# Kernel tuning notes

Hardware: AMD Instinct MI355X
Metric: run time of the kernel (lower is better)

Reference implementation:

```python
import jax, jax.numpy as jnp
import numpy as np

N = 50000          # nodes
E = 800000         # edges (avg degree 16)
T = 4              # edge types (edge_attr_dim)
H = 8              # heads
C1 = 16            # state_dim (per-head channels, layer 1)
C2 = 8             # out_dim  (per-head channels, layer 2)
D = 128            # node_attr_dim
NEG = -1e9         # masked-attention logit
LRELU_SLOPE = 0.2  # PyG GATConv default negative_slope


def setup_inputs() -> dict:
    key = jax.random.key(0)
    ks = jax.random.split(key, 12)
    x = jax.random.normal(ks[0], (N, D), jnp.float32)
    edge_src = jax.random.randint(ks[1], (E,), 0, N, jnp.int32)
    edge_dst = jax.random.randint(ks[2], (E,), 0, N, jnp.int32)
    edge_type = jax.random.randint(ks[3], (E,), 0, T, jnp.int32)
    W1 = jax.random.normal(ks[4], (T, D, H * C1), jnp.float32) * (1.0 / np.sqrt(D))
    a1_src = jax.random.normal(ks[5], (T, H, C1), jnp.float32) * 0.1
    a1_dst = jax.random.normal(ks[6], (T, H, C1), jnp.float32) * 0.1
    b1 = jnp.zeros((T, H * C1), jnp.float32)
    W2 = jax.random.normal(ks[7], (T, H * C1, H * C2), jnp.float32) * (1.0 / np.sqrt(H * C1))
    a2_src = jax.random.normal(ks[8], (T, H, C2), jnp.float32) * 0.1
    a2_dst = jax.random.normal(ks[9], (T, H, C2), jnp.float32) * 0.1
    b2 = jnp.zeros((T, H * C2), jnp.float32)
    return dict(x=x, edge_src=edge_src, edge_dst=edge_dst, edge_type=edge_type,
                W1=W1, a1_src=a1_src, a1_dst=a1_dst, b1=b1,
                W2=W2, a2_src=a2_src, a2_dst=a2_dst, b2=b2)


def gat_conv(x_in, W, a_src, a_dst, b, src, dst, mask, n):
    """One PyG-style GATConv (concat heads, eval mode) on masked edge list."""
    heads, c = a_src.shape
    h = (x_in @ W).reshape(n, heads, c)                       # [N,H,C]
    s_src = jnp.sum(h * a_src, axis=-1)                        # [N,H]
    s_dst = jnp.sum(h * a_dst, axis=-1)                        # [N,H]
    e = jax.nn.leaky_relu(s_src[src] + s_dst[dst], LRELU_SLOPE)  # [Et,H]
    e = jnp.where(mask[:, None], e, NEG)
    m = jax.ops.segment_max(e, dst, num_segments=n)            # [N,H]
    p = jnp.exp(e - m[dst]) * mask[:, None].astype(e.dtype)    # unnorm softmax
    denom = jax.ops.segment_sum(p, dst, num_segments=n)        # [N,H]
    msg = p[:, :, None] * h[src]                               # [Et,H,C]
    agg = jax.ops.segment_sum(msg, dst, num_segments=n)        # [N,H,C]
    out = agg / denom[:, :, None]
    return out.reshape(n, heads * c) + b


def reference(x, edge_src, edge_dst, edge_type, W1, a1_src, a1_dst, b1,
              W2, a2_src, a2_dst, b2):
    n = x.shape[0]
    loops = jnp.arange(n, dtype=edge_src.dtype)
    src = jnp.concatenate([edge_src, loops])   # self-loops appended (PyG default)
    dst = jnp.concatenate([edge_dst, loops])
    ones = jnp.ones((n,), bool)
    outs = []
    for t in range(T):
        mask = jnp.concatenate([edge_type == t, ones])
        h1 = gat_conv(x, W1[t], a1_src[t], a1_dst[t], b1[t], src, dst, mask, n)
        h1 = jax.nn.relu(h1)
        h2 = gat_conv(h1, W2[t], a2_src[t], a2_dst[t], b2[t], src, dst, mask, n)
        outs.append(h2)
    return jnp.concatenate(outs, axis=1)       # [N, T*H*C2]
```

## Files before the change

### kernel.cpp

```cpp
#include <hip/hip_runtime.h>
#include <cstddef>

constexpr int NN  = 50000;
constexpr int NE  = 800000;
constexpr int NT  = 4;
constexpr int NH  = 8;
constexpr int C1  = 16;
constexpr int C2  = 8;
constexpr int DD  = 128;
constexpr int HC1 = NH * C1;
constexpr int HC2 = NH * C2;
constexpr int CAP = 22;
constexpr int BSTRIDE = 48;
constexpr float SLOPE = 0.2f;

constexpr int G_ZERO = 2344;
constexpr int G_P1   = NT * 16384 / 256;
constexpr int G_P2   = NT * 8192 / 256;
constexpr int G_SCAT = 782;
constexpr int G_GEMM = (NN + 63) / 64;
constexpr int G_GAT1 = NN / 16;
constexpr int G_GAT2 = (NN + 31) / 32;

using short8 = __attribute__((ext_vector_type(8))) short;
using f32x4  = __attribute__((ext_vector_type(4))) float;
typedef unsigned short u16;
typedef unsigned char  u8;

__device__ __forceinline__ float lrelu(float x) { return x > 0.f ? x : SLOPE * x; }
__device__ __forceinline__ float bfl(unsigned u) { return __uint_as_float(u << 16); }
__device__ __forceinline__ float bfh(unsigned u) { return __uint_as_float(u & 0xffff0000u); }
__device__ __forceinline__ u16 f2bf(float f) {
    unsigned u = __float_as_uint(f);
    return (u16)((u + 0x7fffu + ((u >> 16) & 1u)) >> 16);
}
__device__ __forceinline__ void deci8(uint2 v, float sc, float f[8]) {
    int w0 = (int)v.x, w1 = (int)v.y;
    f[0] = (float)((w0 << 24) >> 24) * sc;
    f[1] = (float)((w0 << 16) >> 24) * sc;
    f[2] = (float)((w0 <<  8) >> 24) * sc;
    f[3] = (float)( w0        >> 24) * sc;
    f[4] = (float)((w1 << 24) >> 24) * sc;
    f[5] = (float)((w1 << 16) >> 24) * sc;
    f[6] = (float)((w1 <<  8) >> 24) * sc;
    f[7] = (float)( w1        >> 24) * sc;
}
__device__ __forceinline__ float dotf(const float h[8], const float* a) {
    return h[0]*a[0] + h[1]*a[1] + h[2]*a[2] + h[3]*a[3]
         + h[4]*a[4] + h[5]*a[5] + h[6]*a[6] + h[7]*a[7];
}
__device__ __forceinline__ float dot8(uint4 hv, const float* a) {
    return bfl(hv.x) * a[0] + bfh(hv.x) * a[1] + bfl(hv.y) * a[2] + bfh(hv.y) * a[3]
         + bfl(hv.z) * a[4] + bfh(hv.z) * a[5] + bfl(hv.w) * a[6] + bfh(hv.w) * a[7];
}
__device__ __forceinline__ unsigned qperm(unsigned own, unsigned part, unsigned sel) {
    return __builtin_amdgcn_perm(own, part, sel);
}

__device__ __forceinline__ void scatter4(int e0, const int* __restrict__ esrc,
        const int* __restrict__ edst, const int* __restrict__ etyp,
        unsigned* __restrict__ bkt, int tmin, int tmax) {
    int bk[4], src[4];
    bool v[4];
    #pragma unroll
    for (int k = 0; k < 4; ++k) {
        int i = e0 + k * 256;
        bk[k] = 0; src[k] = 0;
        v[k] = false;
        if (i < NE) {
            int ty = etyp[i];
            v[k] = (ty >= tmin) && (ty <= tmax);
            if (v[k]) { bk[k] = ty * NN + edst[i]; src[k] = esrc[i]; }
        }
    }
    int slot[4];
    #pragma unroll
    for (int k = 0; k < 4; ++k)
        if (v[k]) slot[k] = atomicAdd((int*)((char*)bkt + (size_t)bk[k] * BSTRIDE), 1);
    #pragma unroll
    for (int k = 0; k < 4; ++k)
        if (v[k] && slot[k] < CAP)
            ((u16*)((char*)bkt + (size_t)bk[k] * BSTRIDE))[2 + slot[k]] = (u16)src[k];
}

__global__ __launch_bounds__(256) void init_kernel(const float* __restrict__ W1,
        u16* __restrict__ wp1, const float* __restrict__ W2, u16* __restrict__ wp2,
        unsigned* __restrict__ bkt) {
    const int b = blockIdx.x, tid = threadIdx.x;
    if (b < G_ZERO) {
        int i = b * 256 + tid;
        if (i < 600000) reinterpret_cast<uint4*>(bkt)[i] = make_uint4(0, 0, 0, 0);
    } else if (b < G_ZERO + G_P1) {
        int i = (b - G_ZERO) * 256 + tid;
        int t = i >> 14, r = i & 16383;
        int ntl = r >> 11, ks = (r >> 9) & 3, lane = (r >> 3) & 63, j = r & 7;
        int col = ntl * 16 + (lane & 15);
        int k   = ks * 32 + (lane >> 4) * 8 + j;
        wp1[i] = f2bf(W1[((size_t)t * DD + k) * HC1 + col]);
    } else {
        int i = (b - G_ZERO - G_P1) * 256 + tid;
        int t = i >> 13, r = i & 8191;
        int ntl = r >> 11, ks = (r >> 9) & 3, lane = (r >> 3) & 63, j = r & 7;
        int col = ntl * 16 + (lane & 15);
        int k   = ks * 32 + (lane >> 4) * 8 + j;
        wp2[i] = f2bf(W2[((size_t)t * HC1 + k) * HC2 + col]);
    }
}

__global__ __launch_bounds__(256) void scat_kernel(const int* __restrict__ esrc,
        const int* __restrict__ edst, const int* __restrict__ etyp,
        unsigned* __restrict__ bkt, int t) {
    scatter4(blockIdx.x * 1024 + threadIdx.x, esrc, edst, etyp, bkt, t, t);
}

__global__ __launch_bounds__(256) void gemm_kernel(const float* __restrict__ x,
        const u16* __restrict__ wp1, u8* __restrict__ h1, float* __restrict__ sc1) {
    constexpr int NTILE = HC1 / 16;
    const int bx = blockIdx.x, tid = threadIdx.x;
    const int wave = tid >> 6;
    const int lane = tid & 63;
    const int q    = lane >> 4;
    const int c    = lane & 15;
    const int rowbase = bx * 64 + wave * 16;

    int arow = rowbase + c; if (arow >= NN) arow = NN - 1;
    short8 afrag[4];
    const float* xp = x + (size_t)arow * DD + q * 8;
    #pragma unroll
    for (int ks = 0; ks < 4; ++ks) {
        float4 f0 = *reinterpret_cast<const float4*>(xp + ks * 32);
        float4 f1 = *reinterpret_cast<const float4*>(xp + ks * 32 + 4);
        short8 a;
        a[0] = (short)f2bf(f0.x); a[1] = (short)f2bf(f0.y);
        a[2] = (short)f2bf(f0.z); a[3] = (short)f2bf(f0.w);
        a[4] = (short)f2bf(f1.x); a[5] = (short)f2bf(f1.y);
        a[6] = (short)f2bf(f1.z); a[7] = (short)f2bf(f1.w);
        afrag[ks] = a;
    }

    for (int t = 0; t < 4; ++t) {
        f32x4 acc[NTILE];
        #pragma unroll
        for (int ntl = 0; ntl < NTILE; ++ntl) acc[ntl] = (f32x4){0.f, 0.f, 0.f, 0.f};
        const short8* wp = reinterpret_cast<const short8*>(wp1 + (size_t)t * 16384) + lane;
        #pragma unroll
        for (int ntl = 0; ntl < NTILE; ++ntl)
            #pragma unroll
            for (int ks = 0; ks < 4; ++ks) {
                short8 b = wp[(ntl * 4 + ks) * 64];
                acc[ntl] = __builtin_amdgcn_mfma_f32_16x16x32_bf16(afrag[ks], b, acc[ntl], 0, 0, 0);
            }

        float mx[NTILE][4];
        #pragma unroll
        for (int ntl = 0; ntl < NTILE; ++ntl)
            #pragma unroll
            for (int reg = 0; reg < 4; ++reg) mx[ntl][reg] = fabsf(acc[ntl][reg]);
        #pragma unroll
        for (int m = 1; m < 16; m <<= 1)
            #pragma unroll
            for (int ntl = 0; ntl < NTILE; ++ntl)
                #pragma unroll
                for (int reg = 0; reg < 4; ++reg)
                    mx[ntl][reg] = fmaxf(mx[ntl][reg], __shfl_xor(mx[ntl][reg], m));

        u8*    h1w = h1  + (size_t)t * NN * HC1;
        float* scw = sc1 + (size_t)t * NN * 8;

        #pragma unroll
        for (int reg = 0; reg < 4; ++reg) {
            int row = rowbase + q * 4 + reg;
            unsigned w0 = 0, w1 = 0;
            #pragma unroll
            for (int ntl = 0; ntl < 4; ++ntl) {
                float m = mx[ntl][reg];
                float rs = m > 0.f ? 127.f / m : 0.f;
                int iv = __float2int_rn(acc[ntl][reg] * rs);
                w0 |= ((unsigned)iv & 0xffu) << (8 * ntl);
            }
            #pragma unroll
            for (int ntl = 4; ntl < 8; ++ntl) {
                float m = mx[ntl][reg];
                float rs = m > 0.f ? 127.f / m : 0.f;
                int iv = __float2int_rn(acc[ntl][reg] * rs);
                w1 |= ((unsigned)iv & 0xffu) << (8 * (ntl - 4));
            }
            unsigned sel1 = (c & 1) ? 0x07030501u : 0x02060004u;
            unsigned p0 = __shfl_xor(w0, 1), p1 = __shfl_xor(w1, 1);
            w0 = qperm(w0, p0, sel1);
            w1 = qperm(w1, p1, sel1);
            unsigned sel2 = (c & 2) ? 0x07060302u : 0x01000504u;
            p0 = __shfl_xor(w0, 2); p1 = __shfl_xor(w1, 2);
            w0 = qperm(w0, p0, sel2);
            w1 = qperm(w1, p1, sel2);
            if (row < NN) {
                unsigned* rp = reinterpret_cast<unsigned*>(h1w + (size_t)row * HC1);
                rp[(c & 3) * 4 + (c >> 2)]       = w0;
                rp[((c & 3) + 4) * 4 + (c >> 2)] = w1;
            }
        }
        {
            int reg = c >> 2, hp = c & 3;
            int row = rowbase + q * 4 + reg;
            if (row < NN) {
                float2 s;
                s.x = mx[2 * hp][reg] * (1.f / 127.f);
                s.y = mx[2 * hp + 1][reg] * (1.f / 127.f);
                reinterpret_cast<float2*>(scw)[(size_t)row * 4 + hp] = s;
            }
        }
    }
}

template<int TPN, bool SPLIT, bool I8>
__device__ __forceinline__ void gather_body(const unsigned* __restrict__ bkt, int bk,
        int q, const float* asr, float sdn, const void* __restrict__ hbase,
        const float* __restrict__ scp, float& den, float acc[8]) {
    const uint2* bp = reinterpret_cast<const uint2*>((const char*)bkt + (size_t)bk * BSTRIDE);
    unsigned w[12];
    #pragma unroll
    for (int i = 0; i < 6; ++i) { uint2 u = bp[i]; w[2 * i] = u.x; w[2 * i + 1] = u.y; }
    int deg = (int)w[0]; if (deg > CAP) deg = CAP;
    #pragma unroll
    for (int c = 0; c < 6; ++c) {
        if (c * 4 >= deg) break;
        unsigned lo = w[1 + 2 * c];
        unsigned hi = (c < 5) ? w[2 + 2 * c] : 0u;
        int sv[4] = {(int)(lo & 0xffff), (int)(lo >> 16),
                     (int)(hi & 0xffff), (int)(hi >> 16)};
        #pragma unroll
        for (int j = 0; j < 4; ++j) {
            if (c * 4 + j < deg) {
                int sn = sv[j];
                float hf[8];
                if constexpr (I8) {
                    uint2 hv = reinterpret_cast<const uint2*>(hbase)[(size_t)sn * TPN + q];
                    float sc = scp[(size_t)sn * 8 + (q >> 1)];
                    deci8(hv, sc, hf);
                } else {
                    uint4 hv = reinterpret_cast<const uint4*>(hbase)[(size_t)sn * TPN + q];
                    hf[0] = bfl(hv.x); hf[1] = bfh(hv.x);
                    hf[2] = bfl(hv.y); hf[3] = bfh(hv.y);
                    hf[4] = bfl(hv.z); hf[5] = bfh(hv.z);
                    hf[6] = bfl(hv.w); hf[7] = bfh(hv.w);
                }
                float d = dotf(hf, asr);
                if (SPLIT) d += __shfl_xor(d, 1);
                float pp = __expf(lrelu(d + sdn));
                den += pp;
                #pragma unroll
                for (int i = 0; i < 8; ++i) acc[i] += pp * hf[i];
            }
        }
    }
}

__global__ __launch_bounds__(256) void g1g2_kernel(const unsigned* __restrict__ bkt,
        int t, const u8* __restrict__ h1r, const float* __restrict__ sc1r,
        const float* __restrict__ a1s_t, const float* __restrict__ a1d_t,
        const float* __restrict__ b1t, const u16* __restrict__ wp2t,
        u16* __restrict__ h2w) {
    const int bx = blockIdx.x, tid = threadIdx.x;
    __shared__ u16 lt[16][136];
    const int node0 = bx * 16;
    const int nl    = tid >> 4;
    const int node  = node0 + nl;
    const int q     = tid & 15;
    const int head  = q >> 1;
    const int bk    = t * NN + node;

    float asr[8], adr[8];
    #pragma unroll
    for (int i = 0; i < 8; ++i) {
        asr[i] = a1s_t[head * C1 + (q & 1) * 8 + i];
        adr[i] = a1d_t[head * C1 + (q & 1) * 8 + i];
    }

    uint2 hv = reinterpret_cast<const uint2*>(h1r)[(size_t)node * 16 + q];
    float scn = sc1r[(size_t)node * 8 + head];
    float hs[8];
    deci8(hv, scn, hs);
    float ds = dotf(hs, asr); ds += __shfl_xor(ds, 1);
    float dd = dotf(hs, adr); dd += __shfl_xor(dd, 1);
    const float sdn = dd;

    float p = __expf(lrelu(ds + sdn));
    float den = p;
    float acc[8];
    #pragma unroll
    for (int i = 0; i < 8; ++i) acc[i] = p * hs[i];
    gather_body<16, true, true>(bkt, bk, q, asr, sdn, h1r, sc1r, den, acc);

    float inv = 1.f / den;
    uint4 ov;
    {
        float o[8];
        #pragma unroll
        for (int i = 0; i < 8; ++i)
            o[i] = fmaxf(acc[i] * inv + b1t[q * 8 + i], 0.f);
        ov.x = (unsigned)f2bf(o[0]) | ((unsigned)f2bf(o[1]) << 16);
        ov.y = (unsigned)f2bf(o[2]) | ((unsigned)f2bf(o[3]) << 16);
        ov.z = (unsigned)f2bf(o[4]) | ((unsigned)f2bf(o[5]) << 16);
        ov.w = (unsigned)f2bf(o[6]) | ((unsigned)f2bf(o[7]) << 16);
    }
    *reinterpret_cast<uint4*>(&lt[nl][q * 8]) = ov;
    __syncthreads();

    const int wave = tid >> 6;
    const int lane = tid & 63;
    const int quad = lane >> 4;
    const int c    = lane & 15;
    short8 af[4];
    #pragma unroll
    for (int ks = 0; ks < 4; ++ks)
        af[ks] = *reinterpret_cast<const short8*>(&lt[c][ks * 32 + quad * 8]);
    f32x4 cacc = (f32x4){0.f, 0.f, 0.f, 0.f};
    const short8* wp = reinterpret_cast<const short8*>(wp2t) + lane;
    #pragma unroll
    for (int ks = 0; ks < 4; ++ks)
        cacc = __builtin_amdgcn_mfma_f32_16x16x32_bf16(af[ks], wp[(wave * 4 + ks) * 64], cacc, 0, 0, 0);

    const int col = wave * 16 + c;
    #pragma unroll
    for (int reg = 0; reg < 4; ++reg) {
        int row = node0 + quad * 4 + reg;
        h2w[(size_t)row * HC2 + col] = f2bf(cacc[reg]);
    }
}

__global__ __launch_bounds__(256) void gat2_kernel(const unsigned* __restrict__ bkt,
        int t, const u16* __restrict__ h2r, const float* __restrict__ a2s_t,
        const float* __restrict__ a2d_t, const float* __restrict__ b2t,
        float* __restrict__ out) {
    const int bx = blockIdx.x, tid = threadIdx.x;
    const int node = bx * 32 + (tid >> 3);
    if (node >= NN) return;
    const int q    = tid & 7;
    const int head = q;
    const int bk   = t * NN + node;
    const uint4* __restrict__ h4 = reinterpret_cast<const uint4*>(h2r);

    float asr[8], adr[8];
    #pragma unroll
    for (int i = 0; i < 8; ++i) {
        asr[i] = a2s_t[head * C2 + i];
        adr[i] = a2d_t[head * C2 + i];
    }

    uint4 hv = h4[(size_t)node * 8 + q];
    const float sdn = dot8(hv, adr);
    float p = __expf(lrelu(dot8(hv, asr) + sdn));
    float den = p;
    float acc[8];
    acc[0] = p * bfl(hv.x); acc[1] = p * bfh(hv.x);
    acc[2] = p * bfl(hv.y); acc[3] = p * bfh(hv.y);
    acc[4] = p * bfl(hv.z); acc[5] = p * bfh(hv.z);
    acc[6] = p * bfl(hv.w); acc[7] = p * bfh(hv.w);
    gather_body<8, false, false>(bkt, bk, q, asr, sdn, h2r, nullptr, den, acc);

    float inv = 1.f / den;
    float o[8];
    #pragma unroll
    for (int i = 0; i < 8; ++i) o[i] = acc[i] * inv + b2t[q * 8 + i];
    float* op = out + (size_t)node * (NT * HC2) + t * HC2 + q * 8;
    reinterpret_cast<float4*>(op)[0] = make_float4(o[0], o[1], o[2], o[3]);
    reinterpret_cast<float4*>(op)[1] = make_float4(o[4], o[5], o[6], o[7]);
}

extern "C" void kernel_launch(void* const* d_in, const int* in_sizes, int n_in,
                              void* d_out, int out_size, void* d_ws, size_t ws_size,
                              hipStream_t stream) {
    const float* x    = (const float*)d_in[0];
    const int*   esrc = (const int*)d_in[1];
    const int*   edst = (const int*)d_in[2];
    const int*   etyp = (const int*)d_in[3];
    const float* W1   = (const float*)d_in[4];
    const float* a1s  = (const float*)d_in[5];
    const float* a1d  = (const float*)d_in[6];
    const float* b1   = (const float*)d_in[7];
    const float* W2   = (const float*)d_in[8];
    const float* a2s  = (const float*)d_in[9];
    const float* a2d  = (const float*)d_in[10];
    const float* b2   = (const float*)d_in[11];
    float* out = (float*)d_out;
    char* base = (char*)d_ws;

    u8*    h1  = (u8*)base;
    float* sc1 = (float*)(base + 25600000);
    u16*   h2d[2] = {(u16*)(base + 32000000), (u16*)(base + 38400000)};
    unsigned* bkt = (unsigned*)(base + 44800000);
    u16* wp1 = (u16*)(base + 54400000);
    u16* wp2 = (u16*)(base + 54531072);

    dim3 blk(256);
    hipLaunchKernelGGL(init_kernel, dim3(G_ZERO + G_P1 + G_P2), blk, 0, stream,
                       W1, wp1, W2, wp2, bkt);
    for (int t = 0; t < 4; ++t)
        hipLaunchKernelGGL(scat_kernel, dim3(G_SCAT), blk, 0, stream,
                           esrc, edst, etyp, bkt, t);
    hipLaunchKernelGGL(gemm_kernel, dim3(G_GEMM), blk, 0, stream,
                       x, wp1, h1, sc1);

    auto g1g2 = [&](int t) {
        hipLaunchKernelGGL(g1g2_kernel, dim3(G_GAT1), blk, 0, stream,
                           bkt, t, h1 + (size_t)t * NN * HC1, sc1 + (size_t)t * NN * 8,
                           a1s + t * NH * C1, a1d + t * NH * C1, b1 + t * HC1,
                           wp2 + (size_t)t * 8192, h2d[t & 1]);
    };
    auto gat2 = [&](int t) {
        hipLaunchKernelGGL(gat2_kernel, dim3(G_GAT2), blk, 0, stream,
                           bkt, t, h2d[t & 1], a2s + t * NH * C2, a2d + t * NH * C2,
                           b2 + t * HC2, out);
    };
    g1g2(0); g1g2(1); gat2(0); g1g2(2); gat2(1); g1g2(3); gat2(2); gat2(3);
}
```

Measured before the change: 320.7 us.

## Split GEMM across edge types per wave with LDS-staged x and coalesced int8 stores

The layer-1 projection kernel now handles 16 rows per block, and each of the four waves computes one edge type in parallel. Before, each wave handled 16 rows and looped over all four types. The x tile is converted to bf16 once into shared memory and shared by all waves. Quantized int8 outputs are staged in LDS so each wave writes full 16-byte coalesced stores instead of scattered 4-byte ones. This adds a barrier and LDS traffic, quadruples the block count, and drops the row bounds checks because 50000 is divisible by 16.

```diff
diff --git a/kernel.cpp b/kernel.cpp
--- a/kernel.cpp
+++ b/kernel.cpp
@@ -18,7 +18,7 @@
 constexpr int G_P1   = NT * 16384 / 256;
 constexpr int G_P2   = NT * 8192 / 256;
 constexpr int G_SCAT = 782;
-constexpr int G_GEMM = (NN + 63) / 64;
+constexpr int G_GEMM = NN / 16;
 constexpr int G_GAT1 = NN / 16;
 constexpr int G_GAT2 = (NN + 31) / 32;
 
@@ -116,99 +116,105 @@
 __global__ __launch_bounds__(256) void gemm_kernel(const float* __restrict__ x,
         const u16* __restrict__ wp1, u8* __restrict__ h1, float* __restrict__ sc1) {
     constexpr int NTILE = HC1 / 16;
+    __shared__ u16 xls[16][136];
+    __shared__ unsigned st[4][16][36];
     const int bx = blockIdx.x, tid = threadIdx.x;
-    const int wave = tid >> 6;
+    const int w    = tid >> 6;
     const int lane = tid & 63;
     const int q    = lane >> 4;
     const int c    = lane & 15;
-    const int rowbase = bx * 64 + wave * 16;
-
-    int arow = rowbase + c; if (arow >= NN) arow = NN - 1;
+    const int rowbase = bx * 16;
+
+    {
+        int r = tid >> 4, g8 = tid & 15;
+        const float4* xp = reinterpret_cast<const float4*>(
+            x + (size_t)(rowbase + r) * DD + g8 * 8);
+        float4 f0 = xp[0], f1 = xp[1];
+        uint4 o;
+        o.x = (unsigned)f2bf(f0.x) | ((unsigned)f2bf(f0.y) << 16);
+        o.y = (unsigned)f2bf(f0.z) | ((unsigned)f2bf(f0.w) << 16);
+        o.z = (unsigned)f2bf(f1.x) | ((unsigned)f2bf(f1.y) << 16);
+        o.w = (unsigned)f2bf(f1.z) | ((unsigned)f2bf(f1.w) << 16);
+        *reinterpret_cast<uint4*>(&xls[r][g8 * 8]) = o;
+    }
+    __syncthreads();
+
     short8 afrag[4];
-    const float* xp = x + (size_t)arow * DD + q * 8;
-    #pragma unroll
-    for (int ks = 0; ks < 4; ++ks) {
-        float4 f0 = *reinterpret_cast<const float4*>(xp + ks * 32);
-        float4 f1 = *reinterpret_cast<const float4*>(xp + ks * 32 + 4);
-        short8 a;
-        a[0] = (short)f2bf(f0.x); a[1] = (short)f2bf(f0.y);
-        a[2] = (short)f2bf(f0.z); a[3] = (short)f2bf(f0.w);
-        a[4] = (short)f2bf(f1.x); a[5] = (short)f2bf(f1.y);
-        a[6] = (short)f2bf(f1.z); a[7] = (short)f2bf(f1.w);
-        afrag[ks] = a;
-    }
-
-    for (int t = 0; t < 4; ++t) {
-        f32x4 acc[NTILE];
-        #pragma unroll
-        for (int ntl = 0; ntl < NTILE; ++ntl) acc[ntl] = (f32x4){0.f, 0.f, 0.f, 0.f};
-        const short8* wp = reinterpret_cast<const short8*>(wp1 + (size_t)t * 16384) + lane;
+    #pragma unroll
+    for (int ks = 0; ks < 4; ++ks)
+        afrag[ks] = *reinterpret_cast<const short8*>(&xls[c][q * 8 + ks * 32]);
+
+    f32x4 acc[NTILE];
+    #pragma unroll
+    for (int ntl = 0; ntl < NTILE; ++ntl) acc[ntl] = (f32x4){0.f, 0.f, 0.f, 0.f};
+    const short8* wp = reinterpret_cast<const short8*>(wp1 + (size_t)w * 16384) + lane;
+    #pragma unroll
+    for (int ntl = 0; ntl < NTILE; ++ntl)
+        #pragma unroll
+        for (int ks = 0; ks < 4; ++ks) {
+            short8 b = wp[(ntl * 4 + ks) * 64];
+            acc[ntl] = __builtin_amdgcn_mfma_f32_16x16x32_bf16(afrag[ks], b, acc[ntl], 0, 0, 0);
+        }
+
+    float mx[NTILE][4];
+    #pragma unroll
+    for (int ntl = 0; ntl < NTILE; ++ntl)
+        #pragma unroll
+        for (int reg = 0; reg < 4; ++reg) mx[ntl][reg] = fabsf(acc[ntl][reg]);
+    #pragma unroll
+    for (int m = 1; m < 16; m <<= 1)
         #pragma unroll
         for (int ntl = 0; ntl < NTILE; ++ntl)
             #pragma unroll
-            for (int ks = 0; ks < 4; ++ks) {
-                short8 b = wp[(ntl * 4 + ks) * 64];
-                acc[ntl] = __builtin_amdgcn_mfma_f32_16x16x32_bf16(afrag[ks], b, acc[ntl], 0, 0, 0);
-            }
-
-        float mx[NTILE][4];
-        #pragma unroll
-        for (int ntl = 0; ntl < NTILE; ++ntl)
-            #pragma unroll
-            for (int reg = 0; reg < 4; ++reg) mx[ntl][reg] = fabsf(acc[ntl][reg]);
-        #pragma unroll
-        for (int m = 1; m < 16; m <<= 1)
-            #pragma unroll
-            for (int ntl = 0; ntl < NTILE; ++ntl)
-                #pragma unroll
-                for (int reg = 0; reg < 4; ++reg)
-                    mx[ntl][reg] = fmaxf(mx[ntl][reg], __shfl_xor(mx[ntl][reg], m));
-
-        u8*    h1w = h1  + (size_t)t * NN * HC1;
-        float* scw = sc1 + (size_t)t * NN * 8;
-
-        #pragma unroll
-        for (int reg = 0; reg < 4; ++reg) {
-            int row = rowbase + q * 4 + reg;
-            unsigned w0 = 0, w1 = 0;
-            #pragma unroll
-            for (int ntl = 0; ntl < 4; ++ntl) {
-                float m = mx[ntl][reg];
-                float rs = m > 0.f ? 127.f / m : 0.f;
-                int iv = __float2int_rn(acc[ntl][reg] * rs);
-                w0 |= ((unsigned)iv & 0xffu) << (8 * ntl);
-            }
-            #pragma unroll
-            for (int ntl = 4; ntl < 8; ++ntl) {
-                float m = mx[ntl][reg];
-                float rs = m > 0.f ? 127.f / m : 0.f;
-                int iv = __float2int_rn(acc[ntl][reg] * rs);
-                w1 |= ((unsigned)iv & 0xffu) << (8 * (ntl - 4));
-            }
-            unsigned sel1 = (c & 1) ? 0x07030501u : 0x02060004u;
-            unsigned p0 = __shfl_xor(w0, 1), p1 = __shfl_xor(w1, 1);
-            w0 = qperm(w0, p0, sel1);
-            w1 = qperm(w1, p1, sel1);
-            unsigned sel2 = (c & 2) ? 0x07060302u : 0x01000504u;
-            p0 = __shfl_xor(w0, 2); p1 = __shfl_xor(w1, 2);
-            w0 = qperm(w0, p0, sel2);
-            w1 = qperm(w1, p1, sel2);
-            if (row < NN) {
-                unsigned* rp = reinterpret_cast<unsigned*>(h1w + (size_t)row * HC1);
-                rp[(c & 3) * 4 + (c >> 2)]       = w0;
-                rp[((c & 3) + 4) * 4 + (c >> 2)] = w1;
-            }
+            for (int reg = 0; reg < 4; ++reg)
+                mx[ntl][reg] = fmaxf(mx[ntl][reg], __shfl_xor(mx[ntl][reg], m));
+
+    u8*    h1w = h1  + (size_t)w * NN * HC1;
+    float* scw = sc1 + (size_t)w * NN * 8;
+
+    #pragma unroll
+    for (int reg = 0; reg < 4; ++reg) {
+        unsigned w0 = 0, w1 = 0;
+        #pragma unroll
+        for (int ntl = 0; ntl < 4; ++ntl) {
+            float m = mx[ntl][reg];
+            float rs = m > 0.f ? 127.f / m : 0.f;
+            int iv = __float2int_rn(acc[ntl][reg] * rs);
+            w0 |= ((unsigned)iv & 0xffu) << (8 * ntl);
         }
-        {
-            int reg = c >> 2, hp = c & 3;
-            int row = rowbase + q * 4 + reg;
-            if (row < NN) {
-                float2 s;
-                s.x = mx[2 * hp][reg] * (1.f / 127.f);
-                s.y = mx[2 * hp + 1][reg] * (1.f / 127.f);
-                reinterpret_cast<float2*>(scw)[(size_t)row * 4 + hp] = s;
-            }
+        #pragma unroll
+        for (int ntl = 4; ntl < 8; ++ntl) {
+            float m = mx[ntl][reg];
+            float rs = m > 0.f ? 127.f / m : 0.f;
+            int iv = __float2int_rn(acc[ntl][reg] * rs);
+            w1 |= ((unsigned)iv & 0xffu) << (8 * (ntl - 4));
         }
+        unsigned sel1 = (c & 1) ? 0x07030501u : 0x02060004u;
+        unsigned p0 = __shfl_xor(w0, 1), p1 = __shfl_xor(w1, 1);
+        w0 = qperm(w0, p0, sel1);
+        w1 = qperm(w1, p1, sel1);
+        unsigned sel2 = (c & 2) ? 0x07060302u : 0x01000504u;
+        p0 = __shfl_xor(w0, 2); p1 = __shfl_xor(w1, 2);
+        w0 = qperm(w0, p0, sel2);
+        w1 = qperm(w1, p1, sel2);
+        st[w][q * 4 + reg][(c & 3) * 4 + (c >> 2)]      = w0;
+        st[w][q * 4 + reg][(c & 3) * 4 + (c >> 2) + 16] = w1;
+    }
+    {
+        int r0 = lane >> 3, dw = (lane & 7) * 4;
+        uint4 v0 = *reinterpret_cast<const uint4*>(&st[w][r0][dw]);
+        uint4 v1 = *reinterpret_cast<const uint4*>(&st[w][8 + r0][dw]);
+        uint4* dst = reinterpret_cast<uint4*>(h1w + (size_t)rowbase * HC1);
+        dst[lane]      = v0;
+        dst[64 + lane] = v1;
+    }
+    {
+        int reg = c >> 2, hp = c & 3;
+        int row = rowbase + q * 4 + reg;
+        float2 s;
+        s.x = mx[2 * hp][reg] * (1.f / 127.f);
+        s.y = mx[2 * hp + 1][reg] * (1.f / 127.f);
+        reinterpret_cast<float2*>(scw)[(size_t)row * 4 + hp] = s;
     }
 }
 
```

Result: no change. 323.7 us (+0.9%).
